# Performance work log

Hardware: AMD Instinct MI355X
Metric: run time of the kernel (lower is better)

The kernel has to match this reference:

```python
import jax, jax.numpy as jnp
import numpy as np

N_NODES = 100000
N_EDGES = 1600000
HIDDEN_DIM = 64
EIGS_DIM = 32


def setup_inputs() -> dict:
    key = jax.random.key(0)
    k1, k2, k3, k4, k5 = jax.random.split(key, 5)
    q = jax.random.normal(k1, (N_NODES, HIDDEN_DIM), dtype=jnp.float32)
    k = jax.random.normal(k2, (N_NODES, HIDDEN_DIM), dtype=jnp.float32)
    v = jax.random.normal(k3, (N_NODES, HIDDEN_DIM), dtype=jnp.float32)
    eigs = jax.random.normal(k4, (N_NODES, EIGS_DIM), dtype=jnp.float32)
    lambda0 = jnp.zeros((1,), dtype=jnp.float32)  # nn.Parameter(torch.zeros(1))
    indices = jax.random.randint(k5, (2, N_EDGES), 0, N_NODES, dtype=jnp.int64)
    return {"q": q, "k": k, "v": v, "eigs": eigs, "lambda0": lambda0,
            "indices": indices}


def reference(q, k, v, eigs, lambda0, indices):
    n = q.shape[0]
    inv_sqrt_dim = 1.0 / jnp.sqrt(jnp.asarray(q.shape[1], dtype=q.dtype))
    i0 = indices[0]  # destination/row node per edge
    i1 = indices[1]  # source/col node per edge

    # per-edge attention logits: gather-dot-product
    x = jnp.sum(q[i0] * k[i1], axis=-1) * inv_sqrt_dim          # [E]
    y = jnp.sum(eigs[i0] * eigs[i1], axis=-1)                   # [E]
    s = x + jnp.exp(lambda0[0]) * y                             # [E]

    # sparse softmax: clamp(exp(s), -5, 5) then segment-normalize by row sum
    e = jnp.clip(jnp.exp(s), -5.0, 5.0)                         # [E]
    denom = jax.ops.segment_sum(e, i0, num_segments=n)          # [N]
    denom = jnp.where(denom == 0.0, 1.0, denom)
    w = e / denom[i0]                                           # [E]

    # spmm: out[r] = sum_{edges with row r} w_e * v[col_e]
    out = jax.ops.segment_sum(w[:, None] * v[i1], i0, num_segments=n)  # [N, D]
    return out
```

## Files before the change

### kernel.cpp

```cpp
#include <hip/hip_runtime.h>


#define HD 64
#define ED 32
#define CAP 64
#define RPP 256
#define PSHIFT 8
#define D1 36
#define NB1 256
#define PCAP 5120
#define SPILL_CAP 131072

__global__ void p1_bin_kernel(const int* __restrict__ idx, int n_edges,
                              int NP, int chunk,
                              int* __restrict__ part, int* __restrict__ gcur,
                              long long* __restrict__ spill,
                              int* __restrict__ spill_cnt,
                              int* __restrict__ flag) {
    extern __shared__ int sm[];
    int* cnt  = sm;
    int* bins = sm + NP;
    int tid = threadIdx.x;

    for (int i = tid; i < NP; i += 256) cnt[i] = 0;
    __syncthreads();

    int e0 = blockIdx.x * chunk;
    int n  = n_edges - e0; if (n > chunk) n = chunk; if (n < 0) n = 0;

    for (int i = tid; i < n; i += 256) {
        int e = e0 + i;
        int r = idx[e];
        int c = idx[n_edges + e];
        int p = r >> PSHIFT;
        int w = ((r & (RPP - 1)) << 17) | c;
        int pos = atomicAdd(&cnt[p], 1);
        if (pos < D1) {
            bins[p * D1 + pos] = w;
        } else {
            int s = atomicAdd(spill_cnt, 1);
            if (s < SPILL_CAP) spill[s] = ((long long)r << 32) | (unsigned)c;
            else *flag = 1;
        }
    }
    __syncthreads();

    for (int p = tid; p < NP; p += 256) {
        int m = cnt[p]; if (m > D1) m = D1;
        if (m > 0) {
            int base = atomicAdd(&gcur[p], m);
            for (int j = 0; j < m; ++j) {
                int slot = base + j;
                int w = bins[p * D1 + j];
                if (slot < PCAP) {
                    part[p * PCAP + slot] = w;
                } else {
                    int r = (p << PSHIFT) | (w >> 17);
                    int c = w & 0x1FFFF;
                    int s = atomicAdd(spill_cnt, 1);
                    if (s < SPILL_CAP) spill[s] = ((long long)r << 32) | (unsigned)c;
                    else *flag = 1;
                }
            }
        }
    }
}

__global__ void p2_bucket_kernel(const int* __restrict__ part,
                                 const int* __restrict__ gcur,
                                 int* __restrict__ count,
                                 int* __restrict__ bucket, int n_nodes) {
    __shared__ int cnt[RPP];
    int tid = threadIdx.x;
    cnt[tid] = 0;
    __syncthreads();

    int p = blockIdx.x;
    int n = gcur[p]; if (n > PCAP) n = PCAP;

    for (int i = tid; i < n; i += 256) {
        int w  = part[p * PCAP + i];
        int rl = w >> 17;
        int c  = w & 0x1FFFF;
        int pos = atomicAdd(&cnt[rl], 1);
        if (pos < CAP) {
            long long r = (long long)((p << PSHIFT) + rl);
            bucket[r * CAP + pos] = c;
        }
    }
    __syncthreads();

    int r = (p << PSHIFT) + tid;
    if (r < n_nodes) count[r] = cnt[tid];
}

__global__ void spill_drain_kernel(const long long* __restrict__ spill,
                                   const int* __restrict__ spill_cnt,
                                   int* __restrict__ count,
                                   int* __restrict__ bucket) {
    int ns = *spill_cnt; if (ns > SPILL_CAP) ns = SPILL_CAP;
    int stride = gridDim.x * blockDim.x;
    for (int t = blockIdx.x * blockDim.x + threadIdx.x; t < ns; t += stride) {
        long long wc = spill[t];
        int r = (int)(wc >> 32);
        int c = (int)(wc & 0xFFFFFFFFLL);
        int pos = atomicAdd(&count[r], 1);
        if (pos < CAP) bucket[(long long)r * CAP + pos] = c;
    }
}

__global__ void repair_zero_kernel(const int* __restrict__ flag,
                                   int* __restrict__ count, int n_nodes) {
    if (*flag == 0) return;
    int t = blockIdx.x * blockDim.x + threadIdx.x;
    if (t < n_nodes) count[t] = 0;
}

__global__ void repair_scatter_kernel(const int* __restrict__ flag,
                                      const int* __restrict__ idx,
                                      int* __restrict__ count,
                                      int* __restrict__ bucket, int n_edges) {
    if (*flag == 0) return;
    int t = blockIdx.x * blockDim.x + threadIdx.x;
    if (t < n_edges) {
        int r = idx[t];
        int c = idx[n_edges + t];
        int p = atomicAdd(&count[r], 1);
        if (p < CAP) bucket[(long long)r * CAP + p] = c;
    }
}

__global__ void bucket_scatter_kernel(const int* __restrict__ idx,
                                      int* __restrict__ count,
                                      int* __restrict__ bucket, int n_edges) {
    int t = blockIdx.x * blockDim.x + threadIdx.x;
    if (t < n_edges) {
        int r = idx[t];
        int c = idx[n_edges + t];
        int p = atomicAdd(&count[r], 1);
        if (p < CAP) bucket[(long long)r * CAP + p] = c;
    }
}

__global__ void row_kernel(const float* __restrict__ q, const float* __restrict__ k,
                           const float* __restrict__ v, const float* __restrict__ eigs,
                           const float* __restrict__ lambda0,
                           const int* __restrict__ counts,
                           const int* __restrict__ col,
                           const int* __restrict__ idx, int n_edges,
                           float* __restrict__ out, int n_nodes) {
    long long tid = (long long)blockIdx.x * blockDim.x + threadIdx.x;
    int r = (int)(tid >> 6);
    if (r >= n_nodes) return;
    int lane = threadIdx.x & 63;
    int sub = lane & 15;
    int grp = lane >> 4;

    int deg = counts[r];
    const float expL = __expf(lambda0[0]);

    if (deg > CAP) {
        float qs = q[(long long)r * HD + lane] * 0.125f;
        float gs = (lane < ED) ? eigs[(long long)r * ED + lane] * expL : 0.f;
        float accs = 0.f, den = 0.f;
        for (int base = 0; base < n_edges; base += 64) {
            int e = base + lane;
            int rr = (e < n_edges) ? idx[e] : -1;
            int cc = (e < n_edges) ? idx[n_edges + e] : 0;
            unsigned long long mm = __ballot(rr == r);
            while (mm) {
                int b = __ffsll(mm) - 1;
                mm &= mm - 1;
                int c = __shfl(cc, b, 64);
                float kb = k[(long long)c * HD + lane];
                float gb = (lane < ED) ? eigs[(long long)c * ED + lane] : 0.f;
                float s = qs * kb + gs * gb;
                #pragma unroll
                for (int off = 32; off > 0; off >>= 1) s += __shfl_xor(s, off, 64);
                float e1 = fminf(__expf(s), 5.0f);
                den += e1;
                accs += e1 * v[(long long)c * HD + lane];
            }
        }
        float inv = (den == 0.f) ? 1.f : __frcp_rn(den);
        out[(long long)r * HD + lane] = accs * inv;
        return;
    }

    long long start = (long long)r * CAP;

    float4 qa = *(const float4*)(q    + (long long)r * HD + sub * 4);
    float2 ga = *(const float2*)(eigs + (long long)r * ED + sub * 2);
    qa.x *= 0.125f; qa.y *= 0.125f; qa.z *= 0.125f; qa.w *= 0.125f;
    ga.x *= expL;   ga.y *= expL;

    float4 acc = make_float4(0.f, 0.f, 0.f, 0.f);
    float den = 0.f;

    for (int base = 0; base < deg; base += 64) {
        int m = deg - base; if (m > 64) m = 64;
        int cl = (lane < m) ? col[start + base + lane] : 0;
        for (int j = 0; j < m; j += 8) {
            int c1 = __shfl(cl, j + grp,     64);
            int c2 = __shfl(cl, j + 4 + grp, 64);
            float4 kb1 = *(const float4*)(k    + (long long)c1 * HD + sub * 4);
            float2 gb1 = *(const float2*)(eigs + (long long)c1 * ED + sub * 2);
            float4 vv1 = *(const float4*)(v    + (long long)c1 * HD + sub * 4);
            float4 kb2 = *(const float4*)(k    + (long long)c2 * HD + sub * 4);
            float2 gb2 = *(const float2*)(eigs + (long long)c2 * ED + sub * 2);
            float4 vv2 = *(const float4*)(v    + (long long)c2 * HD + sub * 4);

            float s1 = qa.x*kb1.x + qa.y*kb1.y + qa.z*kb1.z + qa.w*kb1.w
                     + ga.x*gb1.x + ga.y*gb1.y;
            float s2 = qa.x*kb2.x + qa.y*kb2.y + qa.z*kb2.z + qa.w*kb2.w
                     + ga.x*gb2.x + ga.y*gb2.y;
            #pragma unroll
            for (int off = 8; off > 0; off >>= 1) {
                s1 += __shfl_xor(s1, off, 64);
                s2 += __shfl_xor(s2, off, 64);
            }
            float e1 = fminf(__expf(s1), 5.0f);
            float e2 = fminf(__expf(s2), 5.0f);

            if (j + grp < m) {
                den += e1;
                acc.x += e1 * vv1.x; acc.y += e1 * vv1.y;
                acc.z += e1 * vv1.z; acc.w += e1 * vv1.w;
            }
            if (j + 4 + grp < m) {
                den += e2;
                acc.x += e2 * vv2.x; acc.y += e2 * vv2.y;
                acc.z += e2 * vv2.z; acc.w += e2 * vv2.w;
            }
        }
    }

    #pragma unroll
    for (int off = 16; off < 64; off <<= 1) {
        acc.x += __shfl_xor(acc.x, off, 64);
        acc.y += __shfl_xor(acc.y, off, 64);
        acc.z += __shfl_xor(acc.z, off, 64);
        acc.w += __shfl_xor(acc.w, off, 64);
        den   += __shfl_xor(den,   off, 64);
    }

    if (grp == 0) {
        float inv = (den == 0.0f) ? 1.0f : __frcp_rn(den);
        float4 o = make_float4(acc.x * inv, acc.y * inv, acc.z * inv, acc.w * inv);
        *(float4*)(out + (long long)r * HD + sub * 4) = o;
    }
}

__global__ void edge_fused_kernel(const float* __restrict__ q,
                                  const float* __restrict__ k,
                                  const float* __restrict__ v,
                                  const float* __restrict__ eigs,
                                  const float* __restrict__ lambda0,
                                  const int* __restrict__ idx,
                                  float* __restrict__ denom,
                                  float* __restrict__ out, int n_edges) {
    long long gid = (long long)blockIdx.x * blockDim.x + threadIdx.x;
    int lane = threadIdx.x & 63;
    int edge = (int)(gid >> 4);
    int sub  = (int)(gid & 15);
    int valid = (edge < n_edges);
    int ec = valid ? edge : (n_edges - 1);
    int i0 = idx[ec];
    int i1 = idx[n_edges + ec];
    const float expL = __expf(lambda0[0]);
    float4 qa = *(const float4*)(q + (long long)i0 * HD + sub * 4);
    float4 kb = *(const float4*)(k + (long long)i1 * HD + sub * 4);
    float c = (qa.x*kb.x + qa.y*kb.y + qa.z*kb.z + qa.w*kb.w) * 0.125f;
    float2 ea = *(const float2*)(eigs + (long long)i0 * ED + sub * 2);
    float2 eb = *(const float2*)(eigs + (long long)i1 * ED + sub * 2);
    c += expL * (ea.x * eb.x + ea.y * eb.y);
    #pragma unroll
    for (int off = 8; off > 0; off >>= 1) c += __shfl_xor(c, off, 64);
    float e = fminf(__expf(c), 5.0f);
    if (valid && sub == 0) atomicAdd(&denom[i0], e);
    #pragma unroll
    for (int j = 0; j < 4; ++j) {
        float ej = __shfl(e,     j * 16, 64);
        int   r  = __shfl(i0,    j * 16, 64);
        int   s  = __shfl(i1,    j * 16, 64);
        int   vj = __shfl(valid, j * 16, 64);
        if (vj) {
            float vv = v[(long long)s * HD + lane];
            atomicAdd(&out[(long long)r * HD + lane], ej * vv);
        }
    }
}

__global__ void normalize_kernel(float* __restrict__ out,
                                 const float* __restrict__ denom, int n_nodes) {
    int t = blockIdx.x * blockDim.x + threadIdx.x;
    int total = n_nodes * (HD / 4);
    if (t >= total) return;
    int row = t >> 4;
    float d = denom[row];
    float inv = (d == 0.0f) ? 1.0f : __frcp_rn(d);
    float4* o4 = (float4*)out;
    float4 x = o4[t];
    x.x *= inv; x.y *= inv; x.z *= inv; x.w *= inv;
    o4[t] = x;
}

extern "C" void kernel_launch(void* const* d_in, const int* in_sizes, int n_in,
                              void* d_out, int out_size, void* d_ws, size_t ws_size,
                              hipStream_t stream) {
    const float* q       = (const float*)d_in[0];
    const float* k       = (const float*)d_in[1];
    const float* v       = (const float*)d_in[2];
    const float* eigs    = (const float*)d_in[3];
    const float* lambda0 = (const float*)d_in[4];
    const int*   idx     = (const int*)d_in[5];

    const int n_edges = in_sizes[5] / 2;
    const int n_nodes = in_sizes[0] / HD;

    const int NP = (n_nodes + RPP - 1) / RPP;
    const int eb = (n_edges + 255) / 256;
    long long rthreads = (long long)n_nodes * 64;
    const int rb = (int)((rthreads + 255) / 256);

    size_t need1 = ((size_t)n_nodes + (size_t)n_nodes * CAP
                    + (size_t)NP * PCAP + NP + 2) * sizeof(int)
                 + (size_t)SPILL_CAP * sizeof(long long);
    size_t need2 = ((size_t)n_nodes + (size_t)n_nodes * CAP) * sizeof(int);

    if (ws_size >= need1) {
        int* count     = (int*)d_ws;
        int* bucket    = count + n_nodes;
        int* part      = bucket + (size_t)n_nodes * CAP;
        int* gcur      = part + (size_t)NP * PCAP;
        int* spill_cnt = gcur + NP;
        int* flag      = spill_cnt + 1;
        long long* spill = (long long*)(flag + 1);

        hipMemsetAsync(gcur, 0, (size_t)(NP + 2) * sizeof(int), stream);

        int chunk = (n_edges + NB1 - 1) / NB1;
        size_t smbytes = (size_t)NP * (1 + D1) * sizeof(int);
        p1_bin_kernel<<<NB1, 256, smbytes, stream>>>(idx, n_edges, NP, chunk,
                                                     part, gcur, spill,
                                                     spill_cnt, flag);
        p2_bucket_kernel<<<NP, 256, 0, stream>>>(part, gcur, count, bucket,
                                                 n_nodes);
        spill_drain_kernel<<<256, 256, 0, stream>>>(spill, spill_cnt, count,
                                                    bucket);
        repair_zero_kernel<<<(n_nodes + 255) / 256, 256, 0, stream>>>(flag, count,
                                                                      n_nodes);
        repair_scatter_kernel<<<eb, 256, 0, stream>>>(flag, idx, count, bucket,
                                                      n_edges);
        row_kernel<<<rb, 256, 0, stream>>>(q, k, v, eigs, lambda0, count, bucket,
                                           idx, n_edges, (float*)d_out, n_nodes);
    } else if (ws_size >= need2) {
        int* count  = (int*)d_ws;
        int* bucket = count + n_nodes;
        hipMemsetAsync(count, 0, (size_t)n_nodes * sizeof(int), stream);
        bucket_scatter_kernel<<<eb, 256, 0, stream>>>(idx, count, bucket, n_edges);
        row_kernel<<<rb, 256, 0, stream>>>(q, k, v, eigs, lambda0, count, bucket,
                                           idx, n_edges, (float*)d_out, n_nodes);
    } else {
        float* denom = (float*)d_ws;
        hipMemsetAsync(denom, 0, (size_t)n_nodes * sizeof(float), stream);
        hipMemsetAsync(d_out, 0, (size_t)out_size * sizeof(float), stream);
        long long threads = (long long)n_edges * 16;
        int grid = (int)((threads + 255) / 256);
        edge_fused_kernel<<<grid, 256, 0, stream>>>(q, k, v, eigs, lambda0, idx,
                                                    denom, (float*)d_out, n_edges);
        int n4 = n_nodes * (HD / 4);
        normalize_kernel<<<(n4 + 255) / 256, 256, 0, stream>>>((float*)d_out,
                                                               denom, n_nodes);
    }
}
```

Before: 299.2 us.

## Stage bucket rows in LDS per half-partition and unroll row gather loop deeper

The bucketing kernel now launches two blocks per partition, each handling 128 rows. Each block builds its rows' column lists in a 32KB shared-memory window and then writes them to global memory as coalesced int4 stores, replacing scattered 4-byte global writes. Each block must now read the whole partition and discard half of it, and the large LDS footprint may lower occupancy. Separately, the row kernel's neighbor loop processes four edges per group per iteration instead of two, which puts more gathers in flight at the cost of more registers.

After: 297.5 us. Within noise of the previous version (-0.6%).

```diff
diff --git a/kernel.cpp b/kernel.cpp
--- a/kernel.cpp
+++ b/kernel.cpp
@@ -70,28 +70,37 @@
                                  const int* __restrict__ gcur,
                                  int* __restrict__ count,
                                  int* __restrict__ bucket, int n_nodes) {
-    __shared__ int cnt[RPP];
+    __shared__ int cnt[RPP / 2];
+    __shared__ int win[(RPP / 2) * CAP];
     int tid = threadIdx.x;
-    cnt[tid] = 0;
+    if (tid < RPP / 2) cnt[tid] = 0;
     __syncthreads();
 
-    int p = blockIdx.x;
+    int p    = blockIdx.x >> 1;
+    int half = blockIdx.x & 1;
     int n = gcur[p]; if (n > PCAP) n = PCAP;
 
     for (int i = tid; i < n; i += 256) {
         int w  = part[p * PCAP + i];
         int rl = w >> 17;
+        if ((rl >> 7) != half) continue;
+        int rh = rl & 127;
         int c  = w & 0x1FFFF;
-        int pos = atomicAdd(&cnt[rl], 1);
-        if (pos < CAP) {
-            long long r = (long long)((p << PSHIFT) + rl);
-            bucket[r * CAP + pos] = c;
-        }
+        int pos = atomicAdd(&cnt[rh], 1);
+        if (pos < CAP) win[(rh << 6) + pos] = c;
     }
     __syncthreads();
 
-    int r = (p << PSHIFT) + tid;
-    if (r < n_nodes) count[r] = cnt[tid];
+    int r0 = (p << PSHIFT) + (half << 7);
+    int rows = n_nodes - r0;
+    if (rows > RPP / 2) rows = RPP / 2;
+    if (rows > 0) {
+        int nint4 = rows * (CAP / 4);
+        int4* dst = (int4*)(bucket + (long long)r0 * CAP);
+        const int4* src = (const int4*)win;
+        for (int i = tid; i < nint4; i += 256) dst[i] = src[i];
+        if (tid < rows) count[r0 + tid] = cnt[tid];
+    }
 }
 
 __global__ void spill_drain_kernel(const long long* __restrict__ spill,
@@ -200,27 +209,43 @@
     for (int base = 0; base < deg; base += 64) {
         int m = deg - base; if (m > 64) m = 64;
         int cl = (lane < m) ? col[start + base + lane] : 0;
-        for (int j = 0; j < m; j += 8) {
-            int c1 = __shfl(cl, j + grp,     64);
-            int c2 = __shfl(cl, j + 4 + grp, 64);
+        for (int j = 0; j < m; j += 16) {
+            int c1 = __shfl(cl, j + grp,      64);
+            int c2 = __shfl(cl, j + 4 + grp,  64);
+            int c3 = __shfl(cl, j + 8 + grp,  64);
+            int c4 = __shfl(cl, j + 12 + grp, 64);
             float4 kb1 = *(const float4*)(k    + (long long)c1 * HD + sub * 4);
             float2 gb1 = *(const float2*)(eigs + (long long)c1 * ED + sub * 2);
             float4 vv1 = *(const float4*)(v    + (long long)c1 * HD + sub * 4);
             float4 kb2 = *(const float4*)(k    + (long long)c2 * HD + sub * 4);
             float2 gb2 = *(const float2*)(eigs + (long long)c2 * ED + sub * 2);
             float4 vv2 = *(const float4*)(v    + (long long)c2 * HD + sub * 4);
+            float4 kb3 = *(const float4*)(k    + (long long)c3 * HD + sub * 4);
+            float2 gb3 = *(const float2*)(eigs + (long long)c3 * ED + sub * 2);
+            float4 vv3 = *(const float4*)(v    + (long long)c3 * HD + sub * 4);
+            float4 kb4 = *(const float4*)(k    + (long long)c4 * HD + sub * 4);
+            float2 gb4 = *(const float2*)(eigs + (long long)c4 * ED + sub * 2);
+            float4 vv4 = *(const float4*)(v    + (long long)c4 * HD + sub * 4);
 
             float s1 = qa.x*kb1.x + qa.y*kb1.y + qa.z*kb1.z + qa.w*kb1.w
                      + ga.x*gb1.x + ga.y*gb1.y;
             float s2 = qa.x*kb2.x + qa.y*kb2.y + qa.z*kb2.z + qa.w*kb2.w
                      + ga.x*gb2.x + ga.y*gb2.y;
+            float s3 = qa.x*kb3.x + qa.y*kb3.y + qa.z*kb3.z + qa.w*kb3.w
+                     + ga.x*gb3.x + ga.y*gb3.y;
+            float s4 = qa.x*kb4.x + qa.y*kb4.y + qa.z*kb4.z + qa.w*kb4.w
+                     + ga.x*gb4.x + ga.y*gb4.y;
             #pragma unroll
             for (int off = 8; off > 0; off >>= 1) {
                 s1 += __shfl_xor(s1, off, 64);
                 s2 += __shfl_xor(s2, off, 64);
+                s3 += __shfl_xor(s3, off, 64);
+                s4 += __shfl_xor(s4, off, 64);
             }
             float e1 = fminf(__expf(s1), 5.0f);
             float e2 = fminf(__expf(s2), 5.0f);
+            float e3 = fminf(__expf(s3), 5.0f);
+            float e4 = fminf(__expf(s4), 5.0f);
 
             if (j + grp < m) {
                 den += e1;
@@ -231,6 +256,16 @@
                 den += e2;
                 acc.x += e2 * vv2.x; acc.y += e2 * vv2.y;
                 acc.z += e2 * vv2.z; acc.w += e2 * vv2.w;
+            }
+            if (j + 8 + grp < m) {
+                den += e3;
+                acc.x += e3 * vv3.x; acc.y += e3 * vv3.y;
+                acc.z += e3 * vv3.z; acc.w += e3 * vv3.w;
+            }
+            if (j + 12 + grp < m) {
+                den += e4;
+                acc.x += e4 * vv4.x; acc.y += e4 * vv4.y;
+                acc.z += e4 * vv4.z; acc.w += e4 * vv4.w;
             }
         }
     }
@@ -344,8 +379,8 @@
         p1_bin_kernel<<<NB1, 256, smbytes, stream>>>(idx, n_edges, NP, chunk,
                                                      part, gcur, spill,
                                                      spill_cnt, flag);
-        p2_bucket_kernel<<<NP, 256, 0, stream>>>(part, gcur, count, bucket,
-                                                 n_nodes);
+        p2_bucket_kernel<<<2 * NP, 256, 0, stream>>>(part, gcur, count, bucket,
+                                                     n_nodes);
         spill_drain_kernel<<<256, 256, 0, stream>>>(spill, spill_cnt, count,
                                                     bucket);
         repair_zero_kernel<<<(n_nodes + 255) / 256, 256, 0, stream>>>(flag, count,
```
